# Kernel tuning notes

Measured on AMD Instinct MI355X. Metric: run time of the kernel, lower is better.

Reference implementation:

```python
import jax, jax.numpy as jnp
import numpy as np

N_NODES = 100000
N_EDGES = 3200000
IN_F, HID, N_CLS = 10, 64, 10
NEG_SLOPE = 0.01  # torch default for F.leaky_relu


def gcn_conv(h, src, dst, W, b, n_nodes):
    h = h @ W  # transform first (small feature dim -> cheap)
    # self loops
    loop = jnp.arange(n_nodes, dtype=src.dtype)
    s = jnp.concatenate([src, loop])
    d = jnp.concatenate([dst, loop])
    deg = jax.ops.segment_sum(jnp.ones_like(d, dtype=h.dtype), d, num_segments=n_nodes)
    dinv = jnp.where(deg > 0, jax.lax.rsqrt(deg), 0.0)
    norm = dinv[s] * dinv[d]  # [E+N]
    msg = h[s] * norm[:, None]  # gather + scale
    out = jax.ops.segment_sum(msg, d, num_segments=n_nodes)  # scatter-add
    return out + b


def setup_inputs() -> dict:
    key = jax.random.key(0)
    ks = jax.random.split(key, 10)
    x = jax.random.normal(ks[0], (N_NODES, IN_F), dtype=jnp.float32)
    edge_index = jax.random.randint(ks[1], (2, N_EDGES), 0, N_NODES, dtype=jnp.int64)
    def glorot(k, fan_in, fan_out):
        lim = np.sqrt(6.0 / (fan_in + fan_out))
        return jax.random.uniform(k, (fan_in, fan_out), jnp.float32, -lim, lim)
    W1 = glorot(ks[2], IN_F, HID)
    b1 = jnp.zeros((HID,), jnp.float32)
    W2 = glorot(ks[3], HID, HID)
    b2 = jnp.zeros((HID,), jnp.float32)
    W3 = glorot(ks[4], HID, HID)
    b3 = jnp.zeros((HID,), jnp.float32)
    Wfc = glorot(ks[5], HID, N_CLS)
    bfc = jnp.zeros((N_CLS,), jnp.float32)
    return {"x": x, "edge_index": edge_index, "W1": W1, "b1": b1,
            "W2": W2, "b2": b2, "W3": W3, "b3": b3, "Wfc": Wfc, "bfc": bfc}


def reference(x, edge_index, W1, b1, W2, b2, W3, b3, Wfc, bfc):
    src, dst = edge_index[0], edge_index[1]
    n = x.shape[0]
    h = jax.nn.leaky_relu(gcn_conv(x, src, dst, W1, b1, n), NEG_SLOPE)
    h = jax.nn.leaky_relu(gcn_conv(h, src, dst, W2, b2, n), NEG_SLOPE)
    h = jax.nn.leaky_relu(gcn_conv(h, src, dst, W3, b3, n), NEG_SLOPE)
    return h @ Wfc + bfc
```

## Files before the change

kernel.cpp:

```cpp
#include <hip/hip_runtime.h>
#include <hip/hip_fp16.h>

#define N_NODES_C 100000
#define N_EDGES_C 3200000
#define IN_F_C 10
#define HID_C 64
#define N_CLS_C 10
#define NEG_SLOPE_C 0.01f

#define NBUCK 98
#define BCAP  36864
#define TILE  2048

__global__ __launch_bounds__(256) void k_bucket(const int* __restrict__ src,
                                                const int* __restrict__ dst,
                                                int* __restrict__ bcur,
                                                int* __restrict__ pairs, int E) {
    __shared__ int lcnt[NBUCK];
    __shared__ int gbase[NBUCK];
    const int t = threadIdx.x;
    for (int i = t; i < NBUCK; i += 256) lcnt[i] = 0;
    __syncthreads();
    const int base = blockIdx.x * TILE;
    int p[8], r[8], nb[8];
#pragma unroll
    for (int i = 0; i < 8; ++i) {
        int e = base + t + i * 256;
        if (e < E) {
            int s = src[e], d = dst[e];
            int b = d >> 10;
            nb[i] = b;
            p[i] = (s << 10) | (d & 1023);
            r[i] = atomicAdd(&lcnt[b], 1);
        }
    }
    __syncthreads();
    for (int i = t; i < NBUCK; i += 256)
        gbase[i] = lcnt[i] ? atomicAdd(&bcur[i], lcnt[i]) : 0;
    __syncthreads();
#pragma unroll
    for (int i = 0; i < 8; ++i) {
        int e = base + t + i * 256;
        if (e < E) {
            int pos = gbase[nb[i]] + r[i];
            if (pos < BCAP) pairs[nb[i] * BCAP + pos] = p[i];
        }
    }
}

__global__ __launch_bounds__(128) void k_bscan(const int* __restrict__ bcur,
                                               int* __restrict__ bOff, int nbk) {
    __shared__ int s[128];
    int t = threadIdx.x;
    int v = (t < nbk) ? bcur[t] : 0;
    s[t] = v;
    __syncthreads();
    for (int off = 1; off < 128; off <<= 1) {
        int u = (t >= off) ? s[t - off] : 0;
        __syncthreads();
        s[t] += u;
        __syncthreads();
    }
    if (t < nbk) bOff[t] = s[t] - v;
}

__global__ __launch_bounds__(1024) void k_build(const int* __restrict__ pairs,
                                                const int* __restrict__ bcur,
                                                const int* __restrict__ bOff,
                                                int* __restrict__ row_ptr,
                                                float* __restrict__ dinv,
                                                int* __restrict__ col) {
    __shared__ int hist[1024];
    __shared__ int sm[1024];
    const int b = blockIdx.x;
    const int t = threadIdx.x;
    const int n = min(bcur[b], BCAP);
    const int base = bOff[b];
    const int* pp = pairs + b * BCAP;

    hist[t] = 0;
    __syncthreads();
    for (int i = t; i < n; i += 1024) atomicAdd(&hist[pp[i] & 1023], 1);
    __syncthreads();
    int c = hist[t];
    sm[t] = c;
    __syncthreads();
    for (int off = 1; off < 1024; off <<= 1) {
        int u = (t >= off) ? sm[t - off] : 0;
        __syncthreads();
        sm[t] += u;
        __syncthreads();
    }
    int rp = base + sm[t] - c;
    int gnode = (b << 10) + t;
    if (gnode < N_NODES_C) {
        row_ptr[gnode] = rp;
        dinv[gnode] = rsqrtf((float)(c + 1));
        if (gnode == N_NODES_C - 1) row_ptr[N_NODES_C] = rp + c;
    }
    __syncthreads();
    sm[t] = rp;
    __syncthreads();
    for (int i = t; i < n; i += 1024) {
        int p = pp[i];
        int idx = atomicAdd(&sm[p & 1023], 1);
        col[idx] = p >> 10;
    }
}

__global__ __launch_bounds__(256) void k_mm0(const float* __restrict__ x,
                                             const float* __restrict__ W,
                                             const float* __restrict__ dinv,
                                             __half* __restrict__ hs, int n) {
    __shared__ float4 W4[IN_F_C * 16];
    const int t = threadIdx.x;
    for (int i = t; i < IN_F_C * 16; i += 256) {
        int k = i >> 4, f4 = i & 15;
        W4[i] = ((const float4*)(W + k * HID_C))[f4];
    }
    __syncthreads();
    int idx = blockIdx.x * 256 + t;
    if (idx >= n * 16) return;
    int nn = idx >> 4, f4 = idx & 15;
    const float* row = x + nn * IN_F_C;
    float4 acc = make_float4(0.f, 0.f, 0.f, 0.f);
#pragma unroll
    for (int k = 0; k < IN_F_C; ++k) {
        float xv = row[k];
        float4 w = W4[k * 16 + f4];
        acc.x += xv * w.x; acc.y += xv * w.y; acc.z += xv * w.z; acc.w += xv * w.w;
    }
    float di = dinv[nn];
    ((__half2*)hs)[(nn << 5) + 2 * f4]     = __floats2half2_rn(acc.x * di, acc.y * di);
    ((__half2*)hs)[(nn << 5) + 2 * f4 + 1] = __floats2half2_rn(acc.z * di, acc.w * di);
}

__global__ __launch_bounds__(256) void k_gather16(const int* __restrict__ row_ptr,
                                                  const int* __restrict__ col,
                                                  const __half2* __restrict__ hs,
                                                  const float* __restrict__ dinv,
                                                  const float* __restrict__ b,
                                                  __half* __restrict__ act, int n) {
    const int lane = threadIdx.x & 63;
    const int half = lane >> 5;
    const int fl   = lane & 31;
    const int d = (blockIdx.x << 2) + (threadIdx.x >> 6);
    if (d >= n) return;
    const int beg = row_ptr[d];
    const int end = row_ptr[d + 1];
    float2 acc = make_float2(0.f, 0.f);
    if (!half) {
        float2 v = __half22float2(hs[(d << 5) + fl]);
        acc.x = v.x; acc.y = v.y;
    }
    int e = beg;
    for (; e + 7 < end; e += 8) {
        int i0 = e + half, i1 = e + 2 + half, i2 = e + 4 + half, i3 = e + 6 + half;
        int s0 = col[i0], s1 = col[i1], s2 = col[i2], s3 = col[i3];
        float2 v0 = __half22float2(hs[(s0 << 5) + fl]);
        float2 v1 = __half22float2(hs[(s1 << 5) + fl]);
        float2 v2 = __half22float2(hs[(s2 << 5) + fl]);
        float2 v3 = __half22float2(hs[(s3 << 5) + fl]);
        acc.x += v0.x + v1.x + v2.x + v3.x;
        acc.y += v0.y + v1.y + v2.y + v3.y;
    }
    for (; e < end; e += 2) {
        int i = e + half;
        if (i < end) {
            float2 v = __half22float2(hs[(col[i] << 5) + fl]);
            acc.x += v.x; acc.y += v.y;
        }
    }
    acc.x += __shfl_xor(acc.x, 32, 64);
    acc.y += __shfl_xor(acc.y, 32, 64);
    if (!half) {
        float di = dinv[d];
        float2 bb = ((const float2*)b)[fl];
        float vx = acc.x * di + bb.x;
        float vy = acc.y * di + bb.y;
        vx = vx > 0.f ? vx : NEG_SLOPE_C * vx;
        vy = vy > 0.f ? vy : NEG_SLOPE_C * vy;
        ((__half2*)act)[(d << 5) + fl] = __floats2half2_rn(vx, vy);
    }
}

__global__ __launch_bounds__(256) void k_xform(const __half* __restrict__ act,
                                               const float* __restrict__ W,
                                               const float* __restrict__ dinv,
                                               __half* __restrict__ hs, int n) {
    __shared__ float Ast[HID_C][68];
    __shared__ float4 Wq[HID_C * 16];
    const int t = threadIdx.x;
    const int base = blockIdx.x * 64;

    for (int i = t; i < HID_C * 16; i += 256) Wq[i] = ((const float4*)W)[i];

    {
        const float2* aF2 = (const float2*)act;
        int j = t & 63, qg = t >> 6;
#pragma unroll
        for (int qq = 0; qq < 4; ++qq) {
            int q = qg * 4 + qq;
            int node = base + j;
            float2 raw = make_float2(0.f, 0.f);
            if (node < n) raw = aF2[node * 16 + q];
            __half2* hp = (__half2*)&raw;
            float2 lo = __half22float2(hp[0]);
            float2 hi = __half22float2(hp[1]);
            Ast[4 * q + 0][j] = lo.x;
            Ast[4 * q + 1][j] = lo.y;
            Ast[4 * q + 2][j] = hi.x;
            Ast[4 * q + 3][j] = hi.y;
        }
    }
    __syncthreads();

    const int f4 = t & 15, j4 = t >> 4;
    float4 s0 = make_float4(0.f,0.f,0.f,0.f), s1 = s0, s2 = s0, s3 = s0;
#pragma unroll
    for (int k = 0; k < HID_C; ++k) {
        float4 w = Wq[k * 16 + f4];
        float4 a = *(const float4*)&Ast[k][4 * j4];
        s0.x += a.x * w.x; s0.y += a.x * w.y; s0.z += a.x * w.z; s0.w += a.x * w.w;
        s1.x += a.y * w.x; s1.y += a.y * w.y; s1.z += a.y * w.z; s1.w += a.y * w.w;
        s2.x += a.z * w.x; s2.y += a.z * w.y; s2.z += a.z * w.z; s2.w += a.z * w.w;
        s3.x += a.w * w.x; s3.y += a.w * w.y; s3.z += a.w * w.z; s3.w += a.w * w.w;
    }
    float4 sv[4] = {s0, s1, s2, s3};
#pragma unroll
    for (int jj = 0; jj < 4; ++jj) {
        int node = base + 4 * j4 + jj;
        if (node < n) {
            float di = dinv[node];
            ((__half2*)hs)[(node << 5) + 2 * f4]     = __floats2half2_rn(sv[jj].x * di, sv[jj].y * di);
            ((__half2*)hs)[(node << 5) + 2 * f4 + 1] = __floats2half2_rn(sv[jj].z * di, sv[jj].w * di);
        }
    }
}

__global__ __launch_bounds__(256) void k_fc(const __half* __restrict__ act,
                                            const float* __restrict__ W,
                                            const float* __restrict__ b,
                                            float* __restrict__ out, int n) {
    __shared__ float Wf[HID_C * N_CLS_C];
    const int t = threadIdx.x;
    for (int i = t; i < HID_C * N_CLS_C; i += 256) Wf[i] = W[i];
    __syncthreads();
    int node = blockIdx.x * 256 + t;
    if (node >= n) return;
    float s[N_CLS_C];
#pragma unroll
    for (int c = 0; c < N_CLS_C; ++c) s[c] = b[c];
    const float2* aF2 = (const float2*)act;
#pragma unroll
    for (int q = 0; q < 16; ++q) {
        float2 raw = aF2[node * 16 + q];
        __half2* hp = (__half2*)&raw;
        float2 lo = __half22float2(hp[0]);
        float2 hi = __half22float2(hp[1]);
        float a0 = lo.x, a1 = lo.y, a2 = hi.x, a3 = hi.y;
#pragma unroll
        for (int c = 0; c < N_CLS_C; ++c) {
            s[c] += a0 * Wf[(4*q+0)*N_CLS_C + c] + a1 * Wf[(4*q+1)*N_CLS_C + c]
                  + a2 * Wf[(4*q+2)*N_CLS_C + c] + a3 * Wf[(4*q+3)*N_CLS_C + c];
        }
    }
#pragma unroll
    for (int c = 0; c < N_CLS_C; ++c) out[node * N_CLS_C + c] = s[c];
}

extern "C" void kernel_launch(void* const* d_in, const int* in_sizes, int n_in,
                              void* d_out, int out_size, void* d_ws, size_t ws_size,
                              hipStream_t stream) {
    const float* x   = (const float*)d_in[0];
    const int*   ei  = (const int*)d_in[1];
    const float* W1  = (const float*)d_in[2];
    const float* b1  = (const float*)d_in[3];
    const float* W2  = (const float*)d_in[4];
    const float* b2  = (const float*)d_in[5];
    const float* W3  = (const float*)d_in[6];
    const float* b3  = (const float*)d_in[7];
    const float* Wfc = (const float*)d_in[8];
    const float* bfc = (const float*)d_in[9];
    float* out = (float*)d_out;

    const int N = N_NODES_C;
    const int E = N_EDGES_C;
    const int* src = ei;
    const int* dst = ei + E;

    float*  dinv    = (float*)d_ws;
    int*    bcur    = (int*)(dinv + N);
    int*    bOff    = bcur + 128;
    int*    row_ptr = bOff + 128;
    int*    col     = row_ptr + N + 4;
    int*    pairs   = col + E;
    __half* hsA     = (__half*)pairs;
    __half* actB    = (__half*)(pairs + (size_t)NBUCK * BCAP);

    int gN4  = (N + 3) / 4;
    int gM0  = (N * 16 + 255) / 256;
    int gBK  = (E + TILE - 1) / TILE;
    int gXF  = (N + 63) / 64;
    int gFC  = (N + 255) / 256;

    hipMemsetAsync(bcur, 0, 128 * sizeof(int), stream);
    k_bucket<<<gBK, 256, 0, stream>>>(src, dst, bcur, pairs, E);
    k_bscan<<<1, 128, 0, stream>>>(bcur, bOff, NBUCK);
    k_build<<<NBUCK, 1024, 0, stream>>>(pairs, bcur, bOff, row_ptr, dinv, col);

    k_mm0<<<gM0, 256, 0, stream>>>(x, W1, dinv, hsA, N);
    k_gather16<<<gN4, 256, 0, stream>>>(row_ptr, col, (const __half2*)hsA, dinv, b1, actB, N);
    k_xform<<<gXF, 256, 0, stream>>>(actB, W2, dinv, hsA, N);
    k_gather16<<<gN4, 256, 0, stream>>>(row_ptr, col, (const __half2*)hsA, dinv, b2, actB, N);
    k_xform<<<gXF, 256, 0, stream>>>(actB, W3, dinv, hsA, N);
    k_gather16<<<gN4, 256, 0, stream>>>(row_ptr, col, (const __half2*)hsA, dinv, b3, actB, N);
    k_fc<<<gFC, 256, 0, stream>>>(actB, Wfc, bfc, out, N);
}
```

Measured before the change: 492.4 us.

## Partition CSR neighbours by source range for cache-local gathers; rework xform and fc

The CSR build now sorts each node's neighbours into four source-id ranges and records a per-range row pointer. The gather kernel walks all nodes of a wave for one range before moving to the next, so the gathered feature rows stay within a smaller window that fits in cache. Partial sums are kept in LDS across the passes. The xform and fc kernels are rewritten to do one node per wave with half-precision weights held in LDS. The build pays for this by rescanning the bucket four times, and the gather issues more passes with extra LDS traffic.

Result: slower. 589.2 us (+19.6%).

```diff
diff --git a/kernel.cpp b/kernel.cpp
--- a/kernel.cpp
+++ b/kernel.cpp
@@ -11,6 +11,9 @@
 #define NBUCK 98
 #define BCAP  36864
 #define TILE  2048
+#define NRANGE 4
+#define NDW   13
+#define PGB   2048
 
 __global__ __launch_bounds__(256) void k_bucket(const int* __restrict__ src,
                                                 const int* __restrict__ dst,
@@ -67,20 +70,20 @@
 __global__ __launch_bounds__(1024) void k_build(const int* __restrict__ pairs,
                                                 const int* __restrict__ bcur,
                                                 const int* __restrict__ bOff,
-                                                int* __restrict__ row_ptr,
+                                                int* __restrict__ rp2,
                                                 float* __restrict__ dinv,
                                                 int* __restrict__ col) {
     __shared__ int hist[1024];
     __shared__ int sm[1024];
     const int b = blockIdx.x;
     const int t = threadIdx.x;
-    const int n = min(bcur[b], BCAP);
+    const int nE = min(bcur[b], BCAP);
     const int base = bOff[b];
     const int* pp = pairs + b * BCAP;
 
     hist[t] = 0;
     __syncthreads();
-    for (int i = t; i < n; i += 1024) atomicAdd(&hist[pp[i] & 1023], 1);
+    for (int i = t; i < nE; i += 1024) atomicAdd(&hist[pp[i] & 1023], 1);
     __syncthreads();
     int c = hist[t];
     sm[t] = c;
@@ -93,18 +96,25 @@
     }
     int rp = base + sm[t] - c;
     int gnode = (b << 10) + t;
-    if (gnode < N_NODES_C) {
-        row_ptr[gnode] = rp;
+    bool valid = gnode < N_NODES_C;
+    if (valid) {
         dinv[gnode] = rsqrtf((float)(c + 1));
-        if (gnode == N_NODES_C - 1) row_ptr[N_NODES_C] = rp + c;
+        if (gnode == N_NODES_C - 1) rp2[4 * N_NODES_C] = rp + c;
     }
     __syncthreads();
     sm[t] = rp;
-    __syncthreads();
-    for (int i = t; i < n; i += 1024) {
-        int p = pp[i];
-        int idx = atomicAdd(&sm[p & 1023], 1);
-        col[idx] = p >> 10;
+    for (int r = 0; r < NRANGE; ++r) {
+        __syncthreads();
+        if (valid) rp2[(gnode << 2) | r] = sm[t];
+        __syncthreads();
+        for (int i = t; i < nE; i += 1024) {
+            int p = pp[i];
+            int s = p >> 10;
+            if (s / 25000 == r) {
+                int idx = atomicAdd(&sm[p & 1023], 1);
+                col[idx] = s;
+            }
+        }
     }
 }
 
@@ -135,52 +145,84 @@
     ((__half2*)hs)[(nn << 5) + 2 * f4 + 1] = __floats2half2_rn(acc.z * di, acc.w * di);
 }
 
-__global__ __launch_bounds__(256) void k_gather16(const int* __restrict__ row_ptr,
-                                                  const int* __restrict__ col,
-                                                  const __half2* __restrict__ hs,
-                                                  const float* __restrict__ dinv,
-                                                  const float* __restrict__ b,
-                                                  __half* __restrict__ act, int n) {
-    const int lane = threadIdx.x & 63;
+__global__ __launch_bounds__(256, 8) void k_pg(const int* __restrict__ rp2,
+                                               const int* __restrict__ col,
+                                               const __half2* __restrict__ hs,
+                                               const float* __restrict__ dinv,
+                                               const float* __restrict__ bias,
+                                               __half2* __restrict__ act,
+                                               int n) {
+    __shared__ float2 accL[4][NDW][32];
+    const int t = threadIdx.x;
+    const int lane = t & 63;
+    const int wid  = t >> 6;
     const int half = lane >> 5;
     const int fl   = lane & 31;
-    const int d = (blockIdx.x << 2) + (threadIdx.x >> 6);
-    if (d >= n) return;
-    const int beg = row_ptr[d];
-    const int end = row_ptr[d + 1];
-    float2 acc = make_float2(0.f, 0.f);
-    if (!half) {
-        float2 v = __half22float2(hs[(d << 5) + fl]);
-        acc.x = v.x; acc.y = v.y;
-    }
-    int e = beg;
-    for (; e + 7 < end; e += 8) {
-        int i0 = e + half, i1 = e + 2 + half, i2 = e + 4 + half, i3 = e + 6 + half;
-        int s0 = col[i0], s1 = col[i1], s2 = col[i2], s3 = col[i3];
-        float2 v0 = __half22float2(hs[(s0 << 5) + fl]);
-        float2 v1 = __half22float2(hs[(s1 << 5) + fl]);
-        float2 v2 = __half22float2(hs[(s2 << 5) + fl]);
-        float2 v3 = __half22float2(hs[(s3 << 5) + fl]);
-        acc.x += v0.x + v1.x + v2.x + v3.x;
-        acc.y += v0.y + v1.y + v2.y + v3.y;
-    }
-    for (; e < end; e += 2) {
-        int i = e + half;
-        if (i < end) {
-            float2 v = __half22float2(hs[(col[i] << 5) + fl]);
-            acc.x += v.x; acc.y += v.y;
-        }
-    }
-    acc.x += __shfl_xor(acc.x, 32, 64);
-    acc.y += __shfl_xor(acc.y, 32, 64);
-    if (!half) {
-        float di = dinv[d];
-        float2 bb = ((const float2*)b)[fl];
-        float vx = acc.x * di + bb.x;
-        float vy = acc.y * di + bb.y;
-        vx = vx > 0.f ? vx : NEG_SLOPE_C * vx;
-        vy = vy > 0.f ? vy : NEG_SLOPE_C * vy;
-        ((__half2*)act)[(d << 5) + fl] = __floats2half2_rn(vx, vy);
+    const int wave = (blockIdx.x << 2) + wid;
+    const int base = wave * NDW;
+    if (base >= n) return;
+
+    for (int r = 0; r < NRANGE; ++r) {
+        for (int j = 0; j < NDW; ++j) {
+            int d = base + j;
+            if (d >= n) break;
+            int beg = rp2[(d << 2) + r];
+            int end = rp2[(d << 2) + r + 1];
+            float2 acc = make_float2(0.f, 0.f);
+            int e = beg;
+            for (; e + 7 < end; e += 8) {
+                int i0 = e + half, i1 = e + 2 + half, i2 = e + 4 + half, i3 = e + 6 + half;
+                int s0 = col[i0], s1 = col[i1], s2 = col[i2], s3 = col[i3];
+                float2 v0 = __half22float2(hs[(s0 << 5) + fl]);
+                float2 v1 = __half22float2(hs[(s1 << 5) + fl]);
+                float2 v2 = __half22float2(hs[(s2 << 5) + fl]);
+                float2 v3 = __half22float2(hs[(s3 << 5) + fl]);
+                acc.x += v0.x + v1.x + v2.x + v3.x;
+                acc.y += v0.y + v1.y + v2.y + v3.y;
+            }
+            if (e + 3 < end) {
+                int i0 = e + half, i1 = e + 2 + half;
+                int s0 = col[i0], s1 = col[i1];
+                float2 v0 = __half22float2(hs[(s0 << 5) + fl]);
+                float2 v1 = __half22float2(hs[(s1 << 5) + fl]);
+                acc.x += v0.x + v1.x;
+                acc.y += v0.y + v1.y;
+                e += 4;
+            }
+            for (; e < end; e += 2) {
+                int i = e + half;
+                if (i < end) {
+                    float2 v = __half22float2(hs[(col[i] << 5) + fl]);
+                    acc.x += v.x; acc.y += v.y;
+                }
+            }
+            acc.x += __shfl_xor(acc.x, 32, 64);
+            acc.y += __shfl_xor(acc.y, 32, 64);
+            if (!half) {
+                if (r == 0) {
+                    accL[wid][j][fl] = acc;
+                } else {
+                    float2 o = accL[wid][j][fl];
+                    o.x += acc.x; o.y += acc.y;
+                    accL[wid][j][fl] = o;
+                }
+            }
+        }
+    }
+    for (int j = 0; j < NDW; ++j) {
+        int d = base + j;
+        if (d >= n) break;
+        if (!half) {
+            float2 a = accL[wid][j][fl];
+            float2 sv = __half22float2(hs[(d << 5) + fl]);
+            float di = dinv[d];
+            float2 bb = ((const float2*)bias)[fl];
+            float vx = (a.x + sv.x) * di + bb.x;
+            float vy = (a.y + sv.y) * di + bb.y;
+            vx = vx > 0.f ? vx : NEG_SLOPE_C * vx;
+            vy = vy > 0.f ? vy : NEG_SLOPE_C * vy;
+            act[(d << 5) + fl] = __floats2half2_rn(vx, vy);
+        }
     }
 }
 
@@ -188,53 +230,36 @@
                                                const float* __restrict__ W,
                                                const float* __restrict__ dinv,
                                                __half* __restrict__ hs, int n) {
-    __shared__ float Ast[HID_C][68];
-    __shared__ float4 Wq[HID_C * 16];
+    __shared__ uint4 aLDS[64][8];
+    __shared__ __half2 Wh2[32 * 64];
     const int t = threadIdx.x;
     const int base = blockIdx.x * 64;
-
-    for (int i = t; i < HID_C * 16; i += 256) Wq[i] = ((const float4*)W)[i];
-
-    {
-        const float2* aF2 = (const float2*)act;
-        int j = t & 63, qg = t >> 6;
-#pragma unroll
-        for (int qq = 0; qq < 4; ++qq) {
-            int q = qg * 4 + qq;
-            int node = base + j;
-            float2 raw = make_float2(0.f, 0.f);
-            if (node < n) raw = aF2[node * 16 + q];
-            __half2* hp = (__half2*)&raw;
-            float2 lo = __half22float2(hp[0]);
-            float2 hi = __half22float2(hp[1]);
-            Ast[4 * q + 0][j] = lo.x;
-            Ast[4 * q + 1][j] = lo.y;
-            Ast[4 * q + 2][j] = hi.x;
-            Ast[4 * q + 3][j] = hi.y;
-        }
-    }
-    __syncthreads();
-
-    const int f4 = t & 15, j4 = t >> 4;
-    float4 s0 = make_float4(0.f,0.f,0.f,0.f), s1 = s0, s2 = s0, s3 = s0;
-#pragma unroll
-    for (int k = 0; k < HID_C; ++k) {
-        float4 w = Wq[k * 16 + f4];
-        float4 a = *(const float4*)&Ast[k][4 * j4];
-        s0.x += a.x * w.x; s0.y += a.x * w.y; s0.z += a.x * w.z; s0.w += a.x * w.w;
-        s1.x += a.y * w.x; s1.y += a.y * w.y; s1.z += a.y * w.z; s1.w += a.y * w.w;
-        s2.x += a.z * w.x; s2.y += a.z * w.y; s2.z += a.z * w.z; s2.w += a.z * w.w;
-        s3.x += a.w * w.x; s3.y += a.w * w.y; s3.z += a.w * w.z; s3.w += a.w * w.w;
-    }
-    float4 sv[4] = {s0, s1, s2, s3};
-#pragma unroll
-    for (int jj = 0; jj < 4; ++jj) {
-        int node = base + 4 * j4 + jj;
-        if (node < n) {
-            float di = dinv[node];
-            ((__half2*)hs)[(node << 5) + 2 * f4]     = __floats2half2_rn(sv[jj].x * di, sv[jj].y * di);
-            ((__half2*)hs)[(node << 5) + 2 * f4 + 1] = __floats2half2_rn(sv[jj].z * di, sv[jj].w * di);
-        }
+    for (int i = t; i < 32 * 64; i += 256) {
+        int k2 = i >> 6, f = i & 63;
+        Wh2[i] = __floats2half2_rn(W[(2 * k2) * HID_C + f], W[(2 * k2 + 1) * HID_C + f]);
+    }
+    const uint4* aG = (const uint4*)act;
+    for (int i = t; i < 64 * 8; i += 256) {
+        int row = i >> 3, q = i & 7;
+        aLDS[row][q] = aG[(size_t)(base + row) * 8 + q];
+    }
+    __syncthreads();
+
+    const int lane = t & 63;
+    const int wid  = t >> 6;
+#pragma unroll 4
+    for (int ii = 0; ii < 16; ++ii) {
+        int nn = wid * 16 + ii;
+        int node = base + nn;
+        const __half2* aRow = (const __half2*)&aLDS[nn][0];
+        float s = 0.f;
+#pragma unroll
+        for (int k2 = 0; k2 < 32; ++k2) {
+            float2 af = __half22float2(aRow[k2]);
+            float2 wf = __half22float2(Wh2[(k2 << 6) + lane]);
+            s += af.x * wf.x + af.y * wf.y;
+        }
+        if (node < n) hs[((size_t)node << 6) + lane] = __float2half(s * dinv[node]);
     }
 }
 
@@ -242,31 +267,39 @@
                                             const float* __restrict__ W,
                                             const float* __restrict__ b,
                                             float* __restrict__ out, int n) {
-    __shared__ float Wf[HID_C * N_CLS_C];
-    const int t = threadIdx.x;
-    for (int i = t; i < HID_C * N_CLS_C; i += 256) Wf[i] = W[i];
-    __syncthreads();
-    int node = blockIdx.x * 256 + t;
-    if (node >= n) return;
-    float s[N_CLS_C];
-#pragma unroll
-    for (int c = 0; c < N_CLS_C; ++c) s[c] = b[c];
-    const float2* aF2 = (const float2*)act;
-#pragma unroll
-    for (int q = 0; q < 16; ++q) {
-        float2 raw = aF2[node * 16 + q];
-        __half2* hp = (__half2*)&raw;
-        float2 lo = __half22float2(hp[0]);
-        float2 hi = __half22float2(hp[1]);
-        float a0 = lo.x, a1 = lo.y, a2 = hi.x, a3 = hi.y;
-#pragma unroll
-        for (int c = 0; c < N_CLS_C; ++c) {
-            s[c] += a0 * Wf[(4*q+0)*N_CLS_C + c] + a1 * Wf[(4*q+1)*N_CLS_C + c]
-                  + a2 * Wf[(4*q+2)*N_CLS_C + c] + a3 * Wf[(4*q+3)*N_CLS_C + c];
-        }
-    }
-#pragma unroll
-    for (int c = 0; c < N_CLS_C; ++c) out[node * N_CLS_C + c] = s[c];
+    __shared__ uint4 aLDS[64][8];
+    __shared__ float2 Wf2[32 * N_CLS_C];
+    __shared__ float bL[N_CLS_C];
+    const int t = threadIdx.x;
+    const int base = blockIdx.x * 64;
+    for (int i = t; i < 32 * N_CLS_C; i += 256) {
+        int k2 = i / N_CLS_C, c = i - k2 * N_CLS_C;
+        Wf2[i] = make_float2(W[(2 * k2) * N_CLS_C + c], W[(2 * k2 + 1) * N_CLS_C + c]);
+    }
+    if (t < N_CLS_C) bL[t] = b[t];
+    const uint4* aG = (const uint4*)act;
+    for (int i = t; i < 64 * 8; i += 256) {
+        int row = i >> 3, q = i & 7;
+        aLDS[row][q] = aG[(size_t)(base + row) * 8 + q];
+    }
+    __syncthreads();
+
+    const int lane = t & 63;
+    const int wid  = t >> 6;
+    if (lane >= N_CLS_C) return;
+    for (int ii = 0; ii < 16; ++ii) {
+        int nn = wid * 16 + ii;
+        int node = base + nn;
+        const __half2* aRow = (const __half2*)&aLDS[nn][0];
+        float s = bL[lane];
+#pragma unroll
+        for (int k2 = 0; k2 < 32; ++k2) {
+            float2 af = __half22float2(aRow[k2]);
+            float2 wf = Wf2[k2 * N_CLS_C + lane];
+            s += af.x * wf.x + af.y * wf.y;
+        }
+        if (node < n) out[(size_t)node * N_CLS_C + lane] = s;
+    }
 }
 
 extern "C" void kernel_launch(void* const* d_in, const int* in_sizes, int n_in,
@@ -289,31 +322,30 @@
     const int* src = ei;
     const int* dst = ei + E;
 
-    float*  dinv    = (float*)d_ws;
-    int*    bcur    = (int*)(dinv + N);
-    int*    bOff    = bcur + 128;
-    int*    row_ptr = bOff + 128;
-    int*    col     = row_ptr + N + 4;
-    int*    pairs   = col + E;
-    __half* hsA     = (__half*)pairs;
-    __half* actB    = (__half*)(pairs + (size_t)NBUCK * BCAP);
-
-    int gN4  = (N + 3) / 4;
-    int gM0  = (N * 16 + 255) / 256;
-    int gBK  = (E + TILE - 1) / TILE;
-    int gXF  = (N + 63) / 64;
-    int gFC  = (N + 255) / 256;
+    float*  dinv = (float*)d_ws;
+    int*    bcur = (int*)(dinv + N);
+    int*    bOff = bcur + 128;
+    int*    rp2  = bOff + 128;
+    int*    col  = rp2 + 4 * N + 16;
+    int*    pairs = col + E;
+    __half* hsA  = (__half*)pairs;
+    __half* hsB  = (__half*)(pairs + (size_t)NBUCK * BCAP);
+    __half* act  = hsB + (size_t)N * HID_C;
+
+    int gM0 = (N * 16 + 255) / 256;
+    int gBK = (E + TILE - 1) / TILE;
+    int gXF = (N + 63) / 64;
 
     hipMemsetAsync(bcur, 0, 128 * sizeof(int), stream);
     k_bucket<<<gBK, 256, 0, stream>>>(src, dst, bcur, pairs, E);
     k_bscan<<<1, 128, 0, stream>>>(bcur, bOff, NBUCK);
-    k_build<<<NBUCK, 1024, 0, stream>>>(pairs, bcur, bOff, row_ptr, dinv, col);
+    k_build<<<NBUCK, 1024, 0, stream>>>(pairs, bcur, bOff, rp2, dinv, col);
 
     k_mm0<<<gM0, 256, 0, stream>>>(x, W1, dinv, hsA, N);
-    k_gather16<<<gN4, 256, 0, stream>>>(row_ptr, col, (const __half2*)hsA, dinv, b1, actB, N);
-    k_xform<<<gXF, 256, 0, stream>>>(actB, W2, dinv, hsA, N);
-    k_gather16<<<gN4, 256, 0, stream>>>(row_ptr, col, (const __half2*)hsA, dinv, b2, actB, N);
-    k_xform<<<gXF, 256, 0, stream>>>(actB, W3, dinv, hsA, N);
-    k_gather16<<<gN4, 256, 0, stream>>>(row_ptr, col, (const __half2*)hsA, dinv, b3, actB, N);
-    k_fc<<<gFC, 256, 0, stream>>>(actB, Wfc, bfc, out, N);
-}
+    k_pg<<<PGB, 256, 0, stream>>>(rp2, col, (const __half2*)hsA, dinv, b1, (__half2*)act, N);
+    k_xform<<<gXF, 256, 0, stream>>>(act, W2, dinv, hsB, N);
+    k_pg<<<PGB, 256, 0, stream>>>(rp2, col, (const __half2*)hsB, dinv, b2, (__half2*)act, N);
+    k_xform<<<gXF, 256, 0, stream>>>(act, W3, dinv, hsA, N);
+    k_pg<<<PGB, 256, 0, stream>>>(rp2, col, (const __half2*)hsA, dinv, b3, (__half2*)act, N);
+    k_fc<<<gXF, 256, 0, stream>>>(act, Wfc, bfc, out, N);
+}
```
